# Kernel optimization log

Measured on AMD Instinct MI355X. Metric: run time of the kernel, lower is better.

Reference implementation:

```python
import jax, jax.numpy as jnp
import numpy as np

PAD = 0

def setup_inputs() -> dict:
    key = jax.random.key(0)
    k1, k2, k3, k4 = jax.random.split(key, 4)
    B, S, F, V, H, D = 64, 256, 4, 50257, 768, 512
    words = jax.random.randint(k1, (B, S, F), 0, V, dtype=jnp.int64)  # pad_index=0 occurs rarely at random
    E = jax.random.normal(k2, (V, H), dtype=jnp.float32) * 0.02      # stand-in for transformer last_hidden_state producer
    W = jax.random.normal(k3, (H, D), dtype=jnp.float32) * 0.02      # FFN projection weight
    b = jax.random.normal(k4, (D,), dtype=jnp.float32) * 0.02
    return {"words": words, "E": E, "W": W, "b": b}

def reference(words, E, W, b):
    # words: [B, S, F] subword ids; mask out pad subwords
    mask = (words != PAD)                                  # [B,S,F] bool
    sub = E[words] * mask[..., None].astype(E.dtype)       # [B,S,F,H], pads zeroed
    cnt = mask.sum(-1).astype(E.dtype)                     # [B,S] subwords per word
    # segment-mean over the fix_len axis; fully-padded words -> 0 (matches pad_sequence(..., 0))
    word_emb = sub.sum(-2) / jnp.maximum(cnt, 1.0)[..., None]   # [B,S,H]
    word_emb = jnp.where((cnt > 0)[..., None], word_emb, 0.0)
    return word_emb @ W + b                                # [B,S,D]
```

## Files before the change

kernel.cpp:

```cpp
#include <hip/hip_runtime.h>
#include <hip/hip_bf16.h>

#define M_TOT 16384
#define K_TOT 768
#define N_TOT 512

typedef __attribute__((ext_vector_type(8))) __bf16 bf16x8;
typedef __attribute__((ext_vector_type(4))) float f32x4;

static __device__ __forceinline__ ushort f2bf(float x) {
  union { float f; unsigned int u; } v; v.f = x;
  unsigned int r = v.u + 0x7fffu + ((v.u >> 16) & 1u);
  return (ushort)(r >> 16);
}

static __device__ __forceinline__ void load_lds16(const ushort* g, ushort* l) {
  __builtin_amdgcn_global_load_lds(
      (const __attribute__((address_space(1))) void*)g,
      (__attribute__((address_space(3))) void*)l, 16, 0, 0);
}

__global__ __launch_bounds__(256) void prep_kernel(
    const int* __restrict__ words, const float* __restrict__ E,
    const float* __restrict__ W, ushort* __restrict__ A,
    ushort* __restrict__ Wt) {
  const int bid = blockIdx.x;
  const int t = threadIdx.x;
  if (bid < M_TOT / 4) {
    const int row  = bid * 4 + (t >> 6);
    const int lane = t & 63;
    const int4 w4 = *reinterpret_cast<const int4*>(words + (size_t)row * 4);
    const int ids[4] = {w4.x, w4.y, w4.z, w4.w};

    float a[12];
#pragma unroll
    for (int i = 0; i < 12; ++i) a[i] = 0.f;
    float cnt = 0.f;

#pragma unroll
    for (int f = 0; f < 4; ++f) {
      const int id = ids[f];
      const float msk = (id != 0) ? 1.f : 0.f;
      cnt += msk;
      const float4* __restrict__ src =
          reinterpret_cast<const float4*>(E + (size_t)id * K_TOT);
#pragma unroll
      for (int c = 0; c < 3; ++c) {
        const float4 v = src[c * 64 + lane];
        a[c * 4 + 0] += v.x * msk; a[c * 4 + 1] += v.y * msk;
        a[c * 4 + 2] += v.z * msk; a[c * 4 + 3] += v.w * msk;
      }
    }
    const float s = (cnt > 0.f) ? (1.f / cnt) : 0.f;
    ushort* dst = A + (size_t)row * K_TOT;
#pragma unroll
    for (int c = 0; c < 3; ++c) {
      ushort4 o;
      o.x = f2bf(a[c * 4 + 0] * s);
      o.y = f2bf(a[c * 4 + 1] * s);
      o.z = f2bf(a[c * 4 + 2] * s);
      o.w = f2bf(a[c * 4 + 3] * s);
      *reinterpret_cast<ushort4*>(dst + c * 256 + lane * 4) = o;
    }
  } else {
    __shared__ float tile[64][65];
    const int b2 = bid - M_TOT / 4;
    const int k0 = (b2 % (K_TOT / 64)) * 64;
    const int n0 = (b2 / (K_TOT / 64)) * 64;
#pragma unroll
    for (int i = 0; i < 4; ++i) {
      const int idx = t + i * 256;
      const int r = idx >> 4;
      const int c = (idx & 15) * 4;
      const float4 v = *reinterpret_cast<const float4*>(
          W + (size_t)(k0 + r) * N_TOT + n0 + c);
      tile[r][c + 0] = v.x; tile[r][c + 1] = v.y;
      tile[r][c + 2] = v.z; tile[r][c + 3] = v.w;
    }
    __syncthreads();
#pragma unroll
    for (int i = 0; i < 4; ++i) {
      const int idx = t + i * 256;
      const int rn = idx >> 4;
      const int ck = (idx & 15) * 4;
      ushort4 o;
      o.x = f2bf(tile[ck + 0][rn]);
      o.y = f2bf(tile[ck + 1][rn]);
      o.z = f2bf(tile[ck + 2][rn]);
      o.w = f2bf(tile[ck + 3][rn]);
      *reinterpret_cast<ushort4*>(Wt + (size_t)(n0 + rn) * K_TOT + k0 + ck) = o;
    }
  }
}

__global__ __launch_bounds__(256) void gemm_kernel(
    const ushort* __restrict__ A, const ushort* __restrict__ Bt,
    const float* __restrict__ bias, float* __restrict__ out) {
  __shared__ ushort Al[2][128 * 64];
  __shared__ ushort Bl[2][128 * 64];
  const int t    = threadIdx.x;
  const int lane = t & 63;
  const int w    = t >> 6;
  const int bm   = blockIdx.x >> 2;
  const int bn   = blockIdx.x & 3;
  const int wr   = w >> 1;
  const int wc   = w & 1;

  f32x4 acc[4][4];
#pragma unroll
  for (int m = 0; m < 4; ++m)
#pragma unroll
    for (int n = 0; n < 4; ++n) acc[m][n] = (f32x4){0.f, 0.f, 0.f, 0.f};

  const int srow = t >> 3;
  const int sseg = t & 7;
  const ushort* aptr = A  + (size_t)(bm * 128 + srow) * K_TOT + sseg * 8;
  const ushort* bptr = Bt + (size_t)(bn * 128 + srow) * K_TOT + sseg * 8;

#define STAGE(buf, kt)                                                       \
  do {                                                                       \
    _Pragma("unroll") for (int i = 0; i < 4; ++i) {                          \
      load_lds16(aptr + (size_t)i * 32 * K_TOT + (kt) * 64,                  \
                 &Al[buf][(i * 256 + w * 64) * 8]);                          \
      load_lds16(bptr + (size_t)i * 32 * K_TOT + (kt) * 64,                  \
                 &Bl[buf][(i * 256 + w * 64) * 8]);                          \
    }                                                                        \
  } while (0)

  STAGE(0, 0);
  __syncthreads();

  int cur = 0;
  const int NT = K_TOT / 64;
  for (int kt = 0; kt < NT; ++kt) {
    if (kt + 1 < NT) {
      if (cur == 0) STAGE(1, kt + 1); else STAGE(0, kt + 1);
    }
#pragma unroll
    for (int kk = 0; kk < 2; ++kk) {
      bf16x8 af[4], bf_[4];
      const int ks = kk * 4 + (lane >> 4);
      const ushort* Ab = cur ? Al[1] : Al[0];
      const ushort* Bb = cur ? Bl[1] : Bl[0];
#pragma unroll
      for (int m = 0; m < 4; ++m)
        af[m] = *reinterpret_cast<const bf16x8*>(
            &Ab[(wr * 64 + m * 16 + (lane & 15)) * 64 + ks * 8]);
#pragma unroll
      for (int n = 0; n < 4; ++n)
        bf_[n] = *reinterpret_cast<const bf16x8*>(
            &Bb[(wc * 64 + n * 16 + (lane & 15)) * 64 + ks * 8]);
      __builtin_amdgcn_s_setprio(1);
#pragma unroll
      for (int m = 0; m < 4; ++m)
#pragma unroll
        for (int n = 0; n < 4; ++n)
          acc[m][n] = __builtin_amdgcn_mfma_f32_16x16x32_bf16(
              af[m], bf_[n], acc[m][n], 0, 0, 0);
      __builtin_amdgcn_s_setprio(0);
    }
    __syncthreads();
    cur ^= 1;
  }
#undef STAGE

  const int colBase = bn * 128 + wc * 64 + (lane & 15);
  const int rowBase = bm * 128 + wr * 64 + ((lane >> 4) << 2);
#pragma unroll
  for (int n = 0; n < 4; ++n) {
    const float bv = bias[colBase + n * 16];
#pragma unroll
    for (int m = 0; m < 4; ++m) {
#pragma unroll
      for (int j = 0; j < 4; ++j) {
        __builtin_nontemporal_store(
            acc[m][n][j] + bv,
            &out[(size_t)(rowBase + m * 16 + j) * N_TOT + colBase + n * 16]);
      }
    }
  }
}

extern "C" void kernel_launch(void* const* d_in, const int* in_sizes, int n_in,
                              void* d_out, int out_size, void* d_ws,
                              size_t ws_size, hipStream_t stream) {
  const int*   words = (const int*)d_in[0];
  const float* E     = (const float*)d_in[1];
  const float* W     = (const float*)d_in[2];
  const float* b     = (const float*)d_in[3];
  float* out = (float*)d_out;

  ushort* Aws  = (ushort*)d_ws;
  ushort* Wtws = Aws + (size_t)M_TOT * K_TOT;

  hipLaunchKernelGGL(prep_kernel,
                     dim3(M_TOT / 4 + (K_TOT / 64) * (N_TOT / 64)), dim3(256),
                     0, stream, words, E, W, Aws, Wtws);
  hipLaunchKernelGGL(gemm_kernel, dim3((M_TOT / 128) * (N_TOT / 128)),
                     dim3(256), 0, stream, Aws, Wtws, b, out);
}
```

Measured before the change: 61.21 us.

## Fuse embedding gather-mean into GEMM A-tile staging with full-N blocks

The subword gather, masked mean and bf16 conversion move into the GEMM kernel, which loads E rows into registers and writes bf16 A tiles straight to LDS. The bf16 A matrix no longer round-trips through global memory. Each block now covers 64 rows and the full 512-column output, so every row's gather is done once, and W's transpose runs as a separate small kernel. The cost is larger LDS use (two 512x64 B buffers) and register-held gather loads whose latency has to be hidden behind the MFMA work.

```diff
diff --git a/kernel.cpp b/kernel.cpp
--- a/kernel.cpp
+++ b/kernel.cpp
@@ -4,6 +4,8 @@
 #define M_TOT 16384
 #define K_TOT 768
 #define N_TOT 512
+#define BM 64
+#define NT (K_TOT / 64)
 
 typedef __attribute__((ext_vector_type(8))) __bf16 bf16x8;
 typedef __attribute__((ext_vector_type(4))) float f32x4;
@@ -13,6 +15,9 @@
   unsigned int r = v.u + 0x7fffu + ((v.u >> 16) & 1u);
   return (ushort)(r >> 16);
 }
+static __device__ __forceinline__ unsigned pack2(float lo, float hi) {
+  return (unsigned)f2bf(lo) | ((unsigned)f2bf(hi) << 16);
+}
 
 static __device__ __forceinline__ void load_lds16(const ushort* g, ushort* l) {
   __builtin_amdgcn_global_load_lds(
@@ -20,162 +25,178 @@
       (__attribute__((address_space(3))) void*)l, 16, 0, 0);
 }
 
-__global__ __launch_bounds__(256) void prep_kernel(
+__global__ __launch_bounds__(256) void wt_kernel(const float* __restrict__ W,
+                                                 ushort* __restrict__ Wt) {
+  __shared__ float tile[64][65];
+  const int t  = threadIdx.x;
+  const int k0 = blockIdx.x * 64;
+  const int n0 = blockIdx.y * 64;
+#pragma unroll
+  for (int i = 0; i < 4; ++i) {
+    const int idx = t + i * 256;
+    const int r = idx >> 4;
+    const int c = (idx & 15) * 4;
+    const float4 v =
+        *reinterpret_cast<const float4*>(W + (size_t)(k0 + r) * N_TOT + n0 + c);
+    tile[r][c + 0] = v.x; tile[r][c + 1] = v.y;
+    tile[r][c + 2] = v.z; tile[r][c + 3] = v.w;
+  }
+  __syncthreads();
+#pragma unroll
+  for (int i = 0; i < 4; ++i) {
+    const int idx = t + i * 256;
+    const int rn = idx >> 4;
+    const int ck = (idx & 15) * 4;
+    ushort4 o;
+    o.x = f2bf(tile[ck + 0][rn]);
+    o.y = f2bf(tile[ck + 1][rn]);
+    o.z = f2bf(tile[ck + 2][rn]);
+    o.w = f2bf(tile[ck + 3][rn]);
+    *reinterpret_cast<ushort4*>(Wt + (size_t)(n0 + rn) * K_TOT + k0 + ck) = o;
+  }
+}
+
+__global__ __launch_bounds__(512, 2) void fused_kernel(
     const int* __restrict__ words, const float* __restrict__ E,
-    const float* __restrict__ W, ushort* __restrict__ A,
-    ushort* __restrict__ Wt) {
-  const int bid = blockIdx.x;
-  const int t = threadIdx.x;
-  if (bid < M_TOT / 4) {
-    const int row  = bid * 4 + (t >> 6);
-    const int lane = t & 63;
-    const int4 w4 = *reinterpret_cast<const int4*>(words + (size_t)row * 4);
-    const int ids[4] = {w4.x, w4.y, w4.z, w4.w};
-
-    float a[12];
-#pragma unroll
-    for (int i = 0; i < 12; ++i) a[i] = 0.f;
-    float cnt = 0.f;
-
-#pragma unroll
-    for (int f = 0; f < 4; ++f) {
-      const int id = ids[f];
-      const float msk = (id != 0) ? 1.f : 0.f;
-      cnt += msk;
-      const float4* __restrict__ src =
-          reinterpret_cast<const float4*>(E + (size_t)id * K_TOT);
-#pragma unroll
-      for (int c = 0; c < 3; ++c) {
-        const float4 v = src[c * 64 + lane];
-        a[c * 4 + 0] += v.x * msk; a[c * 4 + 1] += v.y * msk;
-        a[c * 4 + 2] += v.z * msk; a[c * 4 + 3] += v.w * msk;
-      }
-    }
-    const float s = (cnt > 0.f) ? (1.f / cnt) : 0.f;
-    ushort* dst = A + (size_t)row * K_TOT;
-#pragma unroll
-    for (int c = 0; c < 3; ++c) {
-      ushort4 o;
-      o.x = f2bf(a[c * 4 + 0] * s);
-      o.y = f2bf(a[c * 4 + 1] * s);
-      o.z = f2bf(a[c * 4 + 2] * s);
-      o.w = f2bf(a[c * 4 + 3] * s);
-      *reinterpret_cast<ushort4*>(dst + c * 256 + lane * 4) = o;
-    }
-  } else {
-    __shared__ float tile[64][65];
-    const int b2 = bid - M_TOT / 4;
-    const int k0 = (b2 % (K_TOT / 64)) * 64;
-    const int n0 = (b2 / (K_TOT / 64)) * 64;
-#pragma unroll
-    for (int i = 0; i < 4; ++i) {
-      const int idx = t + i * 256;
-      const int r = idx >> 4;
-      const int c = (idx & 15) * 4;
-      const float4 v = *reinterpret_cast<const float4*>(
-          W + (size_t)(k0 + r) * N_TOT + n0 + c);
-      tile[r][c + 0] = v.x; tile[r][c + 1] = v.y;
-      tile[r][c + 2] = v.z; tile[r][c + 3] = v.w;
-    }
-    __syncthreads();
-#pragma unroll
-    for (int i = 0; i < 4; ++i) {
-      const int idx = t + i * 256;
-      const int rn = idx >> 4;
-      const int ck = (idx & 15) * 4;
-      ushort4 o;
-      o.x = f2bf(tile[ck + 0][rn]);
-      o.y = f2bf(tile[ck + 1][rn]);
-      o.z = f2bf(tile[ck + 2][rn]);
-      o.w = f2bf(tile[ck + 3][rn]);
-      *reinterpret_cast<ushort4*>(Wt + (size_t)(n0 + rn) * K_TOT + k0 + ck) = o;
-    }
-  }
-}
-
-__global__ __launch_bounds__(256) void gemm_kernel(
-    const ushort* __restrict__ A, const ushort* __restrict__ Bt,
-    const float* __restrict__ bias, float* __restrict__ out) {
-  __shared__ ushort Al[2][128 * 64];
-  __shared__ ushort Bl[2][128 * 64];
+    const ushort* __restrict__ Bt, const float* __restrict__ bias,
+    float* __restrict__ out) {
+  __shared__ ushort Bl[2][N_TOT * 64];
+  __shared__ ushort Al[2][BM * 64];
+  __shared__ int   eoff_l[BM][4];
+  __shared__ float msk_l[BM][4];
+  __shared__ float scl_l[BM];
+
   const int t    = threadIdx.x;
   const int lane = t & 63;
   const int w    = t >> 6;
-  const int bm   = blockIdx.x >> 2;
-  const int bn   = blockIdx.x & 3;
-  const int wr   = w >> 1;
-  const int wc   = w & 1;
-
-  f32x4 acc[4][4];
-#pragma unroll
-  for (int m = 0; m < 4; ++m)
-#pragma unroll
-    for (int n = 0; n < 4; ++n) acc[m][n] = (f32x4){0.f, 0.f, 0.f, 0.f};
-
-  const int srow = t >> 3;
-  const int sseg = t & 7;
-  const ushort* aptr = A  + (size_t)(bm * 128 + srow) * K_TOT + sseg * 8;
-  const ushort* bptr = Bt + (size_t)(bn * 128 + srow) * K_TOT + sseg * 8;
-
-#define STAGE(buf, kt)                                                       \
-  do {                                                                       \
-    _Pragma("unroll") for (int i = 0; i < 4; ++i) {                          \
-      load_lds16(aptr + (size_t)i * 32 * K_TOT + (kt) * 64,                  \
-                 &Al[buf][(i * 256 + w * 64) * 8]);                          \
-      load_lds16(bptr + (size_t)i * 32 * K_TOT + (kt) * 64,                  \
-                 &Bl[buf][(i * 256 + w * 64) * 8]);                          \
-    }                                                                        \
-  } while (0)
-
-  STAGE(0, 0);
+  const int wr   = w >> 2;
+  const int wc   = w & 3;
+  const int bm   = blockIdx.x;
+
+  if (t < BM) {
+    const int4 w4 =
+        *reinterpret_cast<const int4*>(words + (size_t)(bm * BM + t) * 4);
+    const int ids[4] = {w4.x, w4.y, w4.z, w4.w};
+    float cnt = 0.f;
+#pragma unroll
+    for (int f = 0; f < 4; ++f) {
+      eoff_l[t][f] = ids[f] * K_TOT;
+      const float m = (ids[f] != 0) ? 1.f : 0.f;
+      msk_l[t][f] = m;
+      cnt += m;
+    }
+    scl_l[t] = (cnt > 0.f) ? (1.f / cnt) : 0.f;
+  }
   __syncthreads();
 
+  const int sr = t >> 3;
+  const int ss = t & 7;
+  const float4* pf[4];
+#pragma unroll
+  for (int f = 0; f < 4; ++f)
+    pf[f] = reinterpret_cast<const float4*>(E + eoff_l[sr][f] + ss * 8);
+  const float m0 = msk_l[sr][0], m1 = msk_l[sr][1];
+  const float m2 = msk_l[sr][2], m3 = msk_l[sr][3];
+  const float scl = scl_l[sr];
+  const ushort* bB = Bt + (size_t)sr * K_TOT + ss * 8;
+
+  f32x4 acc[2][8];
+#pragma unroll
+  for (int m = 0; m < 2; ++m)
+#pragma unroll
+    for (int n = 0; n < 8; ++n) acc[m][n] = (f32x4){0.f, 0.f, 0.f, 0.f};
+
+  float4 va[8];
+
+#define A_LOAD(kt)                                                           \
+  do {                                                                       \
+    _Pragma("unroll") for (int f = 0; f < 4; ++f) {                          \
+      va[2 * f + 0] = pf[f][(kt) * 16 + 0];                                  \
+      va[2 * f + 1] = pf[f][(kt) * 16 + 1];                                  \
+    }                                                                        \
+  } while (0)
+
+#define STAGE_B(dst, kt)                                                     \
+  do {                                                                       \
+    _Pragma("unroll") for (int i = 0; i < 8; ++i) {                          \
+      load_lds16(bB + (size_t)i * 64 * K_TOT + (kt) * 64,                    \
+                 &(dst)[(i * 512 + w * 64) * 8]);                            \
+    }                                                                        \
+  } while (0)
+
+#define A_MATH(dst)                                                          \
+  do {                                                                       \
+    float s[8];                                                              \
+    _Pragma("unroll") for (int j = 0; j < 4; ++j) {                          \
+      s[j] = (va[0][j] * m0 + va[2][j] * m1 + va[4][j] * m2 + va[6][j] * m3) \
+             * scl;                                                          \
+      s[4 + j] =                                                             \
+          (va[1][j] * m0 + va[3][j] * m1 + va[5][j] * m2 + va[7][j] * m3) *  \
+          scl;                                                               \
+    }                                                                        \
+    uint4 o;                                                                 \
+    o.x = pack2(s[0], s[1]); o.y = pack2(s[2], s[3]);                        \
+    o.z = pack2(s[4], s[5]); o.w = pack2(s[6], s[7]);                        \
+    *reinterpret_cast<uint4*>(&(dst)[sr * 64 + ss * 8]) = o;                 \
+  } while (0)
+
+#define COMPUTE(Ar, Br)                                                      \
+  do {                                                                       \
+    _Pragma("unroll") for (int kk = 0; kk < 2; ++kk) {                       \
+      const int ks = kk * 4 + (lane >> 4);                                   \
+      bf16x8 af[2], bfr[8];                                                  \
+      _Pragma("unroll") for (int m = 0; m < 2; ++m)                          \
+        af[m] = *reinterpret_cast<const bf16x8*>(                            \
+            &(Ar)[(wr * 32 + m * 16 + (lane & 15)) * 64 + ks * 8]);          \
+      _Pragma("unroll") for (int n = 0; n < 8; ++n)                          \
+        bfr[n] = *reinterpret_cast<const bf16x8*>(                           \
+            &(Br)[(wc * 128 + n * 16 + (lane & 15)) * 64 + ks * 8]);         \
+      __builtin_amdgcn_s_setprio(1);                                         \
+      _Pragma("unroll") for (int m = 0; m < 2; ++m)                          \
+        _Pragma("unroll") for (int n = 0; n < 8; ++n)                        \
+          acc[m][n] = __builtin_amdgcn_mfma_f32_16x16x32_bf16(               \
+              af[m], bfr[n], acc[m][n], 0, 0, 0);                            \
+      __builtin_amdgcn_s_setprio(0);                                         \
+    }                                                                        \
+  } while (0)
+
+  A_LOAD(0);
+  STAGE_B(Bl[0], 0);
+  A_MATH(Al[0]);
+  __syncthreads();
+
   int cur = 0;
-  const int NT = K_TOT / 64;
   for (int kt = 0; kt < NT; ++kt) {
+    const ushort* Ar = cur ? Al[1] : Al[0];
+    const ushort* Br = cur ? Bl[1] : Bl[0];
+    ushort* An = cur ? Al[0] : Al[1];
+    ushort* Bn = cur ? Bl[0] : Bl[1];
     if (kt + 1 < NT) {
-      if (cur == 0) STAGE(1, kt + 1); else STAGE(0, kt + 1);
+      A_LOAD(kt + 1);
+      STAGE_B(Bn, kt + 1);
     }
-#pragma unroll
-    for (int kk = 0; kk < 2; ++kk) {
-      bf16x8 af[4], bf_[4];
-      const int ks = kk * 4 + (lane >> 4);
-      const ushort* Ab = cur ? Al[1] : Al[0];
-      const ushort* Bb = cur ? Bl[1] : Bl[0];
-#pragma unroll
-      for (int m = 0; m < 4; ++m)
-        af[m] = *reinterpret_cast<const bf16x8*>(
-            &Ab[(wr * 64 + m * 16 + (lane & 15)) * 64 + ks * 8]);
-#pragma unroll
-      for (int n = 0; n < 4; ++n)
-        bf_[n] = *reinterpret_cast<const bf16x8*>(
-            &Bb[(wc * 64 + n * 16 + (lane & 15)) * 64 + ks * 8]);
-      __builtin_amdgcn_s_setprio(1);
-#pragma unroll
-      for (int m = 0; m < 4; ++m)
-#pragma unroll
-        for (int n = 0; n < 4; ++n)
-          acc[m][n] = __builtin_amdgcn_mfma_f32_16x16x32_bf16(
-              af[m], bf_[n], acc[m][n], 0, 0, 0);
-      __builtin_amdgcn_s_setprio(0);
-    }
+    COMPUTE(Ar, Br);
+    if (kt + 1 < NT) A_MATH(An);
     __syncthreads();
     cur ^= 1;
   }
-#undef STAGE
-
-  const int colBase = bn * 128 + wc * 64 + (lane & 15);
-  const int rowBase = bm * 128 + wr * 64 + ((lane >> 4) << 2);
-#pragma unroll
-  for (int n = 0; n < 4; ++n) {
-    const float bv = bias[colBase + n * 16];
-#pragma unroll
-    for (int m = 0; m < 4; ++m) {
+#undef A_LOAD
+#undef STAGE_B
+#undef A_MATH
+#undef COMPUTE
+
+  const int col  = wc * 128 + (lane & 15);
+  const int row0 = bm * BM + wr * 32 + ((lane >> 4) << 2);
+#pragma unroll
+  for (int n = 0; n < 8; ++n) {
+    const float bv = bias[col + n * 16];
+#pragma unroll
+    for (int m = 0; m < 2; ++m) {
 #pragma unroll
       for (int j = 0; j < 4; ++j) {
         __builtin_nontemporal_store(
             acc[m][n][j] + bv,
-            &out[(size_t)(rowBase + m * 16 + j) * N_TOT + colBase + n * 16]);
+            &out[(size_t)(row0 + m * 16 + j) * N_TOT + col + n * 16]);
       }
     }
   }
@@ -190,12 +211,10 @@
   const float* b     = (const float*)d_in[3];
   float* out = (float*)d_out;
 
-  ushort* Aws  = (ushort*)d_ws;
-  ushort* Wtws = Aws + (size_t)M_TOT * K_TOT;
-
-  hipLaunchKernelGGL(prep_kernel,
-                     dim3(M_TOT / 4 + (K_TOT / 64) * (N_TOT / 64)), dim3(256),
-                     0, stream, words, E, W, Aws, Wtws);
-  hipLaunchKernelGGL(gemm_kernel, dim3((M_TOT / 128) * (N_TOT / 128)),
-                     dim3(256), 0, stream, Aws, Wtws, b, out);
-}
+  ushort* Wtws = (ushort*)d_ws;
+
+  hipLaunchKernelGGL(wt_kernel, dim3(K_TOT / 64, N_TOT / 64), dim3(256), 0,
+                     stream, W, Wtws);
+  hipLaunchKernelGGL(fused_kernel, dim3(M_TOT / BM), dim3(512), 0, stream,
+                     words, E, Wtws, b, out);
+}
```

Result: slower. 63.99 us (+4.5%).
